# Kernel tuning notes

Measured on AMD Instinct MI355X. Metric: run time of the kernel, lower is better.

Reference implementation:

```python
import jax, jax.numpy as jnp
import numpy as np

B, S, D, H, F = 4, 1024, 1024, 16, 4096
DH = D // H
EPS = 1e-6


def _layer_norm(x, gamma, beta):
    # torch LayerNorm here uses unbiased std (ddof=1) and eps added to std
    mean = jnp.mean(x, axis=-1, keepdims=True)
    std = jnp.std(x, axis=-1, keepdims=True, ddof=1)
    return gamma * (x - mean) / (std + EPS) + beta


def _conv1d(x, w, b):
    # x: [B,S,C]; w: [out,in,3]; pad 'both' -> (1,1), same length
    y = jax.lax.conv_general_dilated(
        jnp.transpose(x, (0, 2, 1)), w, window_strides=(1,),
        padding=[(1, 1)], dimension_numbers=('NCH', 'OIH', 'NCH'))
    return jnp.transpose(y, (0, 2, 1)) + b


def setup_inputs() -> dict:
    key = jax.random.key(0)
    ks = jax.random.split(key, 8)
    sD = 1.0 / np.sqrt(D)
    sF = 1.0 / np.sqrt(F)
    return {
        'inputs': jax.random.normal(ks[0], (B, S, D), dtype=jnp.float32),
        'mask': jnp.zeros((B, 1, S), dtype=bool),
        'gamma1': jnp.ones((D,), jnp.float32),
        'beta1': jnp.zeros((D,), jnp.float32),
        'gamma2': jnp.ones((D,), jnp.float32),
        'beta2': jnp.zeros((D,), jnp.float32),
        'Wq': jax.random.normal(ks[1], (D, D), jnp.float32) * sD,
        'Wk': jax.random.normal(ks[2], (D, D), jnp.float32) * sD,
        'Wv': jax.random.normal(ks[3], (D, D), jnp.float32) * sD,
        'Wo': jax.random.normal(ks[4], (D, D), jnp.float32) * sD,
        'conv1_w': jax.random.normal(ks[5], (F, D, 3), jnp.float32) * sD,
        'conv1_b': jnp.zeros((F,), jnp.float32),
        'conv2_w': jax.random.normal(ks[6], (D, F, 3), jnp.float32) * sF,
        'conv2_b': jnp.zeros((D,), jnp.float32),
    }


def reference(inputs, mask, gamma1, beta1, gamma2, beta2, Wq, Wk, Wv, Wo,
              conv1_w, conv1_b, conv2_w, conv2_b):
    x = inputs
    x_norm = _layer_norm(x, gamma1, beta1)
    # projections (torch Linear, no bias): y = x @ W.T
    q = jnp.einsum('bsd,ed->bse', x_norm, Wq).reshape(B, S, H, DH).transpose(0, 2, 1, 3)
    k = jnp.einsum('bsd,ed->bse', x_norm, Wk).reshape(B, S, H, DH).transpose(0, 2, 1, 3)
    v = jnp.einsum('bsd,ed->bse', x_norm, Wv).reshape(B, S, H, DH).transpose(0, 2, 1, 3)
    q = q * (DH ** -0.5)
    logits = jnp.einsum('bhqd,bhkd->bhqk', q, k)  # [B,H,S,S]
    logits = jnp.where(mask[:, None, :, :], jnp.float32(-1e18), logits)
    weights = jax.nn.softmax(logits, axis=-1)
    ctx = jnp.einsum('bhqk,bhkd->bhqd', weights, v)
    ctx = ctx.transpose(0, 2, 1, 3).reshape(B, S, D)
    attn_out = jnp.einsum('bsd,ed->bse', ctx, Wo)
    x = x + attn_out  # layer dropout is identity at eval
    x_norm = _layer_norm(x, gamma2, beta2)
    # FFN 'cc': conv+relu applied after BOTH convs (source bug i<len always true)
    h = jax.nn.relu(_conv1d(x_norm, conv1_w, conv1_b))
    h = jax.nn.relu(_conv1d(h, conv2_w, conv2_b))
    return x + h
```

## Files before the change

### kernel.cpp

```cpp
#include <hip/hip_runtime.h>
#include <stdint.h>
#include <stddef.h>

typedef unsigned short u16;
typedef short short8 __attribute__((ext_vector_type(8)));
typedef float f32x4 __attribute__((ext_vector_type(4)));

#define B_ 4
#define S_ 1024
#define D_ 1024
#define H_ 16
#define F_ 4096
#define M_ 4096

__device__ __forceinline__ u16 f2bf(float f) {
  union { float f; unsigned u; } v; v.f = f;
  unsigned r = v.u + 0x7fffu + ((v.u >> 16) & 1u);
  return (u16)(r >> 16);
}
__device__ __forceinline__ float bf2f(u16 x) {
  union { unsigned u; float f; } v; v.u = ((unsigned)x) << 16; return v.f;
}

__device__ __forceinline__ void gld16(const u16* g, u16* l) {
  __builtin_amdgcn_global_load_lds(
      (__attribute__((address_space(1))) void*)g,
      (__attribute__((address_space(3))) void*)l, 16, 0, 0);
}

__global__ __launch_bounds__(256) void cvt_wqkvo(const float* __restrict__ q,
                                                 const float* __restrict__ k,
                                                 const float* __restrict__ v,
                                                 const float* __restrict__ o,
                                                 u16* __restrict__ d) {
  int i = blockIdx.x * 256 + threadIdx.x;
  int sel = i >> 18;
  const float* s = sel == 0 ? q : sel == 1 ? k : sel == 2 ? v : o;
  float sc = sel == 0 ? 0.125f : 1.0f;
  float4 val = *(const float4*)(s + (size_t)(i & 262143) * 4);
  unsigned lo = (unsigned)f2bf(val.x * sc) | ((unsigned)f2bf(val.y * sc) << 16);
  unsigned hi = (unsigned)f2bf(val.z * sc) | ((unsigned)f2bf(val.w * sc) << 16);
  *(uint2*)(d + (size_t)i * 4) = make_uint2(lo, hi);
}

__global__ __launch_bounds__(256) void pack3(const float* __restrict__ w,
                                             u16* __restrict__ d, int OUT, int IN) {
  int tot = OUT * IN;
  int i = blockIdx.x * blockDim.x + threadIdx.x;
  int stride = gridDim.x * blockDim.x;
  for (; i < tot; i += stride) {
#pragma unroll
    for (int t = 0; t < 3; ++t) d[(size_t)t * tot + i] = f2bf(w[(size_t)i * 3 + t]);
  }
}

__global__ __launch_bounds__(256) void layernorm(const float* __restrict__ x,
                                                 const float* __restrict__ g,
                                                 const float* __restrict__ be,
                                                 u16* __restrict__ out) {
  __shared__ float red[8];
  const int row = blockIdx.x, tid = threadIdx.x;
  const float* xr = x + (size_t)row * D_;
  float4 v = *(const float4*)(xr + tid * 4);
  float s = v.x + v.y + v.z + v.w;
  float q = v.x * v.x + v.y * v.y + v.z * v.z + v.w * v.w;
#pragma unroll
  for (int o = 32; o; o >>= 1) { s += __shfl_xor(s, o); q += __shfl_xor(q, o); }
  const int w = tid >> 6, lane = tid & 63;
  if (lane == 0) { red[w] = s; red[4 + w] = q; }
  __syncthreads();
  s = red[0] + red[1] + red[2] + red[3];
  q = red[4] + red[5] + red[6] + red[7];
  float mean = s * (1.f / 1024.f);
  float var = (q - 1024.f * mean * mean) * (1.f / 1023.f);
  var = fmaxf(var, 0.f);
  float r = 1.f / (sqrtf(var) + 1e-6f);
  const float* vv = &v.x;
  int c = tid * 4;
  unsigned lo = (unsigned)f2bf(g[c + 0] * (vv[0] - mean) * r + be[c + 0]) |
                ((unsigned)f2bf(g[c + 1] * (vv[1] - mean) * r + be[c + 1]) << 16);
  unsigned hi = (unsigned)f2bf(g[c + 2] * (vv[2] - mean) * r + be[c + 2]) |
                ((unsigned)f2bf(g[c + 3] * (vv[3] - mean) * r + be[c + 3]) << 16);
  *(uint2*)(out + (size_t)row * D_ + c) = make_uint2(lo, hi);
}

template <int MODE, int NN, int KK>
__device__ __forceinline__ void stage_half(int kt, int kind, const u16* __restrict__ Ag,
                                           const u16* __restrict__ Bg,
                                           const u16* __restrict__ zrow, int tapf,
                                           int m0, int n0, int tid,
                                           u16* AsB, u16* BsB) {
  const int buf = kt & 1;
  int tap, k0;
  if (MODE == 1) { tap = kt >> 4; k0 = (kt & 15) << 6; }
  else if (MODE == 2) { tap = tapf; k0 = kt << 6; }
  else { tap = 0; k0 = kt << 6; }
  const int gc = (tid & 7) ^ ((tid >> 3) & 7);
  if (kind >= 2) {
#pragma unroll
    for (int j = 0; j < 2; ++j) {
      int r = (kind - 2) * 64 + j * 128 + (tid >> 3);
      const u16* src;
      if (MODE == 0) {
        src = Ag + (size_t)(m0 + r) * KK + k0 + gc * 8;
      } else {
        int srow = (m0 & 1023) + r + tap - 1;
        src = ((unsigned)srow < 1024u)
                  ? Ag + (size_t)((m0 & ~1023) + srow) * KK + k0 + gc * 8
                  : zrow + k0 + gc * 8;
      }
      gld16(src, AsB + buf * 16384 + r * 64 + (tid & 7) * 8);
    }
  } else {
#pragma unroll
    for (int j = 0; j < 2; ++j) {
      int r = kind * 128 + j * 64 + (tid >> 3);
      const u16* src = Bg + (size_t)tap * NN * KK + (size_t)(n0 + r) * KK + k0 + gc * 8;
      gld16(src, BsB + buf * 16384 + r * 64 + (tid & 7) * 8);
    }
  }
}

template <int MODE, int NN, int KK, int NT>
__global__ __launch_bounds__(512, 2) void gemm256(const u16* __restrict__ Ag,
                                                  const u16* __restrict__ Bg,
                                                  const float* __restrict__ bias,
                                                  const u16* __restrict__ zrow,
                                                  u16* __restrict__ Cb) {
  __shared__ u16 As[2][256][64];
  __shared__ u16 Bs[2][256][64];
  const int tid = threadIdx.x;
  const int w = tid >> 6, lane = tid & 63;
  const int wr = w >> 2, wc = w & 3;

  const int bid = blockIdx.x;
  int wgid, mb, nb, tapf = 0;
  if (MODE == 1) wgid = (bid & 7) * 32 + (bid >> 3);
  else           wgid = (bid & 7) * 24 + (bid >> 3);
  if (MODE == 2) {
    mb = wgid & 15;
    int rest = wgid >> 4;
    tapf = rest >> 2;
    nb = rest & 3;
  } else {
    nb = wgid >> 4;
    mb = wgid & 15;
  }
  const int m0 = mb * 256, n0 = nb * 256;

  u16* AsB = &As[0][0][0];
  u16* BsB = &Bs[0][0][0];

  f32x4 acc[8][4] = {};

  stage_half<MODE, NN, KK>(0, 0, Ag, Bg, zrow, tapf, m0, n0, tid, AsB, BsB);
  stage_half<MODE, NN, KK>(0, 1, Ag, Bg, zrow, tapf, m0, n0, tid, AsB, BsB);
  stage_half<MODE, NN, KK>(0, 2, Ag, Bg, zrow, tapf, m0, n0, tid, AsB, BsB);
  stage_half<MODE, NN, KK>(0, 3, Ag, Bg, zrow, tapf, m0, n0, tid, AsB, BsB);
  stage_half<MODE, NN, KK>(1, 0, Ag, Bg, zrow, tapf, m0, n0, tid, AsB, BsB);
  stage_half<MODE, NN, KK>(1, 1, Ag, Bg, zrow, tapf, m0, n0, tid, AsB, BsB);
  stage_half<MODE, NN, KK>(1, 2, Ag, Bg, zrow, tapf, m0, n0, tid, AsB, BsB);
  asm volatile("s_waitcnt vmcnt(6)" ::: "memory");
  __builtin_amdgcn_s_barrier();

  for (int kt = 0; kt < NT; ++kt) {
    const int buf = kt & 1;
    short8 bF[4][2];
#pragma unroll
    for (int q = 0; q < 4; ++q) {
      short8 aF[2][2];
#pragma unroll
      for (int i = 0; i < 2; ++i)
#pragma unroll
        for (int kk = 0; kk < 2; ++kk) {
          int r = wr * 128 + (2 * q + i) * 16 + (lane & 15);
          int c = kk * 4 + (lane >> 4);
          aF[i][kk] = *(const short8*)&As[buf][r][(c ^ (r & 7)) * 8];
        }
      if (q == 0) {
#pragma unroll
        for (int ni = 0; ni < 4; ++ni)
#pragma unroll
          for (int kk = 0; kk < 2; ++kk) {
            int r = wc * 64 + ni * 16 + (lane & 15);
            int c = kk * 4 + (lane >> 4);
            bF[ni][kk] = *(const short8*)&Bs[buf][r][(c ^ (r & 7)) * 8];
          }
      }
      if (q == 0) { if (kt + 1 < NT) stage_half<MODE, NN, KK>(kt + 1, 3, Ag, Bg, zrow, tapf, m0, n0, tid, AsB, BsB); }
      else if (q == 1) { if (kt + 2 < NT) stage_half<MODE, NN, KK>(kt + 2, 0, Ag, Bg, zrow, tapf, m0, n0, tid, AsB, BsB); }
      else if (q == 2) { if (kt + 2 < NT) stage_half<MODE, NN, KK>(kt + 2, 1, Ag, Bg, zrow, tapf, m0, n0, tid, AsB, BsB); }
      else             { if (kt + 2 < NT) stage_half<MODE, NN, KK>(kt + 2, 2, Ag, Bg, zrow, tapf, m0, n0, tid, AsB, BsB); }
      if (q == 1) {
        if (kt + 2 < NT) asm volatile("s_waitcnt vmcnt(10)" ::: "memory");
        else             asm volatile("s_waitcnt vmcnt(0)" ::: "memory");
      } else if (q == 3) {
        if (kt + 2 < NT)      asm volatile("s_waitcnt vmcnt(8)" ::: "memory");
        else if (kt + 1 < NT) asm volatile("s_waitcnt vmcnt(2)" ::: "memory");
      }
      __builtin_amdgcn_s_barrier();
      asm volatile("s_waitcnt lgkmcnt(0)" ::: "memory");
      __builtin_amdgcn_sched_barrier(0);
      __builtin_amdgcn_s_setprio(1);
#pragma unroll
      for (int i = 0; i < 2; ++i)
#pragma unroll
        for (int ni = 0; ni < 4; ++ni)
#pragma unroll
          for (int kk = 0; kk < 2; ++kk)
            acc[2 * q + i][ni] = __builtin_amdgcn_mfma_f32_16x16x32_bf16(
                aF[i][kk], bF[ni][kk], acc[2 * q + i][ni], 0, 0, 0);
      __builtin_amdgcn_s_setprio(0);
      __builtin_amdgcn_s_barrier();
    }
  }

#pragma unroll
  for (int mi = 0; mi < 8; ++mi)
#pragma unroll
    for (int ni = 0; ni < 4; ++ni)
#pragma unroll
      for (int j = 0; j < 4; ++j) {
        int row = m0 + wr * 128 + mi * 16 + (lane >> 4) * 4 + j;
        int col = n0 + wc * 64 + ni * 16 + (lane & 15);
        float v = acc[mi][ni][j];
        if (MODE == 0) {
          Cb[(size_t)row * NN + col] = f2bf(v);
        } else if (MODE == 1) {
          Cb[(size_t)row * NN + col] = f2bf(fmaxf(v + bias[col], 0.f));
        } else {
          Cb[((size_t)tapf * 4096 + row) * NN + col] = f2bf(v);
        }
      }
}

template <int EPI, int NXB>
__global__ __launch_bounds__(256) void gemm_bt(const u16* __restrict__ A,
                                               const u16* __restrict__ Bm,
                                               int N, int K,
                                               void* __restrict__ C,
                                               const float* __restrict__ res) {
  __shared__ u16 As[128 * 64];
  __shared__ u16 Bs[128 * 64];
  const int tid = threadIdx.x;
  const int w = tid >> 6, lane = tid & 63;
  const int bid = blockIdx.x;
  const int idx = bid >> 3;
  const int xb = (bid & 7) * NXB + idx % NXB;
  const int yb = idx / NXB;
  const int m0 = yb * 128, n0 = xb * 128;
  const int wr = w >> 1, wc = w & 1;
  const int lrow = lane >> 3;
  const int swc = (lane & 7) ^ lrow;

  f32x4 acc[4][4] = {};

  for (int k0 = 0; k0 < K; k0 += 64) {
#pragma unroll
    for (int i = 0; i < 4; ++i) {
      int chunk = w * 4 + i;
      int row = chunk * 8 + lrow;
      gld16(A + (size_t)(m0 + row) * K + k0 + swc * 8, &As[chunk * 512]);
      gld16(Bm + (size_t)(n0 + row) * K + k0 + swc * 8, &Bs[chunk * 512]);
    }
    __syncthreads();
#pragma unroll
    for (int kk = 0; kk < 2; ++kk) {
      short8 aF[4], bF[4];
#pragma unroll
      for (int mi = 0; mi < 4; ++mi) {
        int row = wr * 64 + mi * 16 + (lane & 15);
        int ch = (kk * 4 + (lane >> 4)) ^ (row & 7);
        aF[mi] = *(const short8*)&As[row * 64 + ch * 8];
      }
#pragma unroll
      for (int ni = 0; ni < 4; ++ni) {
        int row = wc * 64 + ni * 16 + (lane & 15);
        int ch = (kk * 4 + (lane >> 4)) ^ (row & 7);
        bF[ni] = *(const short8*)&Bs[row * 64 + ch * 8];
      }
#pragma unroll
      for (int mi = 0; mi < 4; ++mi)
#pragma unroll
        for (int ni = 0; ni < 4; ++ni)
          acc[mi][ni] = __builtin_amdgcn_mfma_f32_16x16x32_bf16(aF[mi], bF[ni], acc[mi][ni], 0, 0, 0);
    }
    __syncthreads();
  }

#pragma unroll
  for (int mi = 0; mi < 4; ++mi)
#pragma unroll
    for (int ni = 0; ni < 4; ++ni)
#pragma unroll
      for (int j = 0; j < 4; ++j) {
        int row = m0 + wr * 64 + mi * 16 + (lane >> 4) * 4 + j;
        int col = n0 + wc * 64 + ni * 16 + (lane & 15);
        float v = acc[mi][ni][j];
        if (EPI == 0) ((u16*)C)[(size_t)row * N + col] = f2bf(v);
        else ((float*)C)[(size_t)row * N + col] = v + res[(size_t)row * N + col];
      }
}

__global__ __launch_bounds__(256) void conv2_reduce(const u16* __restrict__ P,
                                                    const float* __restrict__ bias,
                                                    const float* __restrict__ x2,
                                                    float* __restrict__ out) {
  size_t o = ((size_t)blockIdx.x * 256 + threadIdx.x) * 8;
  int col = (int)(o & 1023);
  short8 a = *(const short8*)(P + o);
  short8 b = *(const short8*)(P + 4194304 + o);
  short8 c = *(const short8*)(P + 8388608 + o);
  float4 r0 = *(const float4*)(x2 + o);
  float4 r1 = *(const float4*)(x2 + o + 4);
  float4 b0 = *(const float4*)(bias + col);
  float4 b1 = *(const float4*)(bias + col + 4);
  float4 o0, o1;
  const float* bb0 = &b0.x; const float* bb1 = &b1.x;
  float* p0 = &o0.x; float* p1 = &o1.x;
  const float* rr0 = &r0.x; const float* rr1 = &r1.x;
#pragma unroll
  for (int j = 0; j < 4; ++j) {
    float v = bf2f((u16)a[j]) + bf2f((u16)b[j]) + bf2f((u16)c[j]) + bb0[j];
    p0[j] = rr0[j] + fmaxf(v, 0.f);
  }
#pragma unroll
  for (int j = 0; j < 4; ++j) {
    float v = bf2f((u16)a[4 + j]) + bf2f((u16)b[4 + j]) + bf2f((u16)c[4 + j]) + bb1[j];
    p1[j] = rr1[j] + fmaxf(v, 0.f);
  }
  *(float4*)(out + o) = o0;
  *(float4*)(out + o + 4) = o1;
}

__global__ __launch_bounds__(256) void transpose_v(const u16* __restrict__ QKV,
                                                   u16* __restrict__ Vt) {
  __shared__ u16 T[64][72];
  const int tid = threadIdx.x;
  const int st = blockIdx.x, h = blockIdx.y, b = blockIdx.z;
  const int s0 = st * 64;
#pragma unroll
  for (int i = 0; i < 2; ++i) {
    int u = tid + i * 256;
    int s = u >> 3, c8 = u & 7;
    uint4 val = *(const uint4*)(QKV + (size_t)(b * 1024 + s0 + s) * 3072 + 2048 + h * 64 + c8 * 8);
    const u16* vp = (const u16*)&val;
#pragma unroll
    for (int k = 0; k < 8; ++k) T[s][c8 * 8 + k] = vp[k];
  }
  __syncthreads();
#pragma unroll
  for (int i = 0; i < 2; ++i) {
    int u = tid + i * 256;
    int d = u >> 3, c8 = u & 7;
    u16 tmp[8];
#pragma unroll
    for (int k = 0; k < 8; ++k) tmp[k] = T[c8 * 8 + k][d];
    uint4 o;
    o.x = (unsigned)tmp[0] | ((unsigned)tmp[1] << 16);
    o.y = (unsigned)tmp[2] | ((unsigned)tmp[3] << 16);
    o.z = (unsigned)tmp[4] | ((unsigned)tmp[5] << 16);
    o.w = (unsigned)tmp[6] | ((unsigned)tmp[7] << 16);
    *(uint4*)(Vt + (size_t)((b * 16 + h) * 64 + d) * 1024 + s0 + c8 * 8) = o;
  }
}

__global__ __launch_bounds__(256) void flash_attn(const u16* __restrict__ QKV,
                                                  const u16* __restrict__ Vt,
                                                  u16* __restrict__ Ctx) {
  __shared__ u16 Ks[64 * 64];
  __shared__ u16 Vs[64 * 64];
  __shared__ u16 Ps[4 * 16 * 64];
  const int tid = threadIdx.x;
  const int w = tid >> 6, lane = tid & 63;
  const int qt = blockIdx.x, h = blockIdx.y, b = blockIdx.z;
  const int q0 = qt * 64 + w * 16;
  const int lrow = lane >> 3;
  const int swc = (lane & 7) ^ lrow;

  short8 qF[2];
#pragma unroll
  for (int kk = 0; kk < 2; ++kk)
    qF[kk] = *(const short8*)(QKV + (size_t)(b * 1024 + q0 + (lane & 15)) * 3072 +
                              h * 64 + kk * 32 + (lane >> 4) * 8);

  float m_r[4], l_r[4];
  f32x4 accO[4] = {};
#pragma unroll
  for (int j = 0; j < 4; ++j) { m_r[j] = -1e30f; l_r[j] = 0.f; }

  for (int kt = 0; kt < 16; ++kt) {
#pragma unroll
    for (int i = 0; i < 2; ++i) {
      int chunk = w * 2 + i;
      int row = chunk * 8 + lrow;
      gld16(QKV + (size_t)(b * 1024 + kt * 64 + row) * 3072 + 1024 + h * 64 + swc * 8,
            &Ks[chunk * 512]);
      gld16(Vt + (size_t)((b * 16 + h) * 64 + row) * 1024 + kt * 64 + swc * 8, &Vs[chunk * 512]);
    }
    __syncthreads();

    f32x4 accS[4] = {};
#pragma unroll
    for (int nt = 0; nt < 4; ++nt) {
#pragma unroll
      for (int kk = 0; kk < 2; ++kk) {
        int row = nt * 16 + (lane & 15);
        int ch = (kk * 4 + (lane >> 4)) ^ (row & 7);
        short8 bF = *(const short8*)&Ks[row * 64 + ch * 8];
        accS[nt] = __builtin_amdgcn_mfma_f32_16x16x32_bf16(qF[kk], bF, accS[nt], 0, 0, 0);
      }
    }

#pragma unroll
    for (int j = 0; j < 4; ++j) {
      float mx = fmaxf(fmaxf(accS[0][j], accS[1][j]), fmaxf(accS[2][j], accS[3][j]));
#pragma unroll
      for (int o = 1; o < 16; o <<= 1) mx = fmaxf(mx, __shfl_xor(mx, o));
      float mnew = fmaxf(m_r[j], mx);
      int prow = (lane >> 4) * 4 + j;
      float s = 0.f;
#pragma unroll
      for (int nt = 0; nt < 4; ++nt) {
        float p = __expf(accS[nt][j] - mnew);
        s += p;
        int col = nt * 16 + (lane & 15);
        int ch = (col >> 3) ^ (prow & 7);
        Ps[w * 1024 + prow * 64 + ch * 8 + (col & 7)] = f2bf(p);
      }
#pragma unroll
      for (int o = 1; o < 16; o <<= 1) s += __shfl_xor(s, o);
      float alpha = __expf(m_r[j] - mnew);
      l_r[j] = l_r[j] * alpha + s;
      m_r[j] = mnew;
#pragma unroll
      for (int nt = 0; nt < 4; ++nt) accO[nt][j] *= alpha;
    }

#pragma unroll
    for (int kk = 0; kk < 2; ++kk) {
      int prow = lane & 15;
      int ch = (kk * 4 + (lane >> 4)) ^ (prow & 7);
      short8 aF = *(const short8*)&Ps[w * 1024 + prow * 64 + ch * 8];
#pragma unroll
      for (int nt = 0; nt < 4; ++nt) {
        int vrow = nt * 16 + (lane & 15);
        int vch = (kk * 4 + (lane >> 4)) ^ (vrow & 7);
        short8 bF = *(const short8*)&Vs[vrow * 64 + vch * 8];
        accO[nt] = __builtin_amdgcn_mfma_f32_16x16x32_bf16(aF, bF, accO[nt], 0, 0, 0);
      }
    }
    __syncthreads();
  }

#pragma unroll
  for (int nt = 0; nt < 4; ++nt)
#pragma unroll
    for (int j = 0; j < 4; ++j) {
      int row = q0 + (lane >> 4) * 4 + j;
      int col = h * 64 + nt * 16 + (lane & 15);
      Ctx[(size_t)(b * 1024 + row) * D_ + col] = f2bf(accO[nt][j] / l_r[j]);
    }
}

extern "C" void kernel_launch(void* const* d_in, const int* in_sizes, int n_in,
                              void* d_out, int out_size, void* d_ws, size_t ws_size,
                              hipStream_t stream) {
  const float* x_in = (const float*)d_in[0];
  const float* g1 = (const float*)d_in[2];
  const float* be1 = (const float*)d_in[3];
  const float* g2 = (const float*)d_in[4];
  const float* be2 = (const float*)d_in[5];
  const float* Wq = (const float*)d_in[6];
  const float* Wk = (const float*)d_in[7];
  const float* Wv = (const float*)d_in[8];
  const float* Wo = (const float*)d_in[9];
  const float* c1w = (const float*)d_in[10];
  const float* c1b = (const float*)d_in[11];
  const float* c2w = (const float*)d_in[12];
  const float* c2b = (const float*)d_in[13];
  float* out = (float*)d_out;
  char* ws = (char*)d_ws;

  const size_t OFF_WQKV = 0;
  const size_t OFF_WOB  = 6291456;
  const size_t OFF_W1T  = 8388608;
  const size_t OFF_W2T  = 33554432;
  const size_t OFF_XN1  = 58720256;
  const size_t OFF_QKV  = 67108864;
  const size_t OFF_H    = OFF_QKV;
  const size_t OFF_VT   = 100663296;
  const size_t OFF_X2   = 109051904;
  const size_t OFF_XN2  = 125829120;
  const size_t OFF_ZROW = 134217728;
  const size_t OFF_P    = 0;
  const size_t NEED     = 134225920;
  if (ws_size < NEED) return;

  u16* wqkv = (u16*)(ws + OFF_WQKV);
  u16* wo_b = (u16*)(ws + OFF_WOB);
  u16* w1t = (u16*)(ws + OFF_W1T);
  u16* w2t = (u16*)(ws + OFF_W2T);
  u16* xn1 = (u16*)(ws + OFF_XN1);
  u16* ctx = xn1;
  u16* qkv = (u16*)(ws + OFF_QKV);
  u16* hbuf = (u16*)(ws + OFF_H);
  u16* vt = (u16*)(ws + OFF_VT);
  float* x2 = (float*)(ws + OFF_X2);
  u16* xn2 = (u16*)(ws + OFF_XN2);
  u16* zrow = (u16*)(ws + OFF_ZROW);
  u16* part = (u16*)(ws + OFF_P);

  hipMemsetAsync(zrow, 0, 8192, stream);

  cvt_wqkvo<<<4096, 256, 0, stream>>>(Wq, Wk, Wv, Wo, wqkv);
  pack3<<<2048, 256, 0, stream>>>(c1w, w1t, F_, D_);
  pack3<<<2048, 256, 0, stream>>>(c2w, w2t, D_, F_);

  layernorm<<<M_, 256, 0, stream>>>(x_in, g1, be1, xn1);

  gemm256<0, 3072, 1024, 16><<<192, 512, 0, stream>>>(xn1, wqkv, nullptr, zrow, qkv);

  transpose_v<<<dim3(16, H_, B_), 256, 0, stream>>>(qkv, vt);

  flash_attn<<<dim3(16, H_, B_), 256, 0, stream>>>(qkv, vt, ctx);

  gemm_bt<1, 1><<<256, 256, 0, stream>>>(ctx, wo_b, 1024, 1024, x2, x_in);

  layernorm<<<M_, 256, 0, stream>>>(x2, g2, be2, xn2);

  gemm256<1, 4096, 1024, 48><<<256, 512, 0, stream>>>(xn2, w1t, c1b, zrow, hbuf);

  gemm256<2, 1024, 4096, 64><<<192, 512, 0, stream>>>(hbuf, w2t, nullptr, zrow, part);
  conv2_reduce<<<2048, 256, 0, stream>>>(part, c2b, x2, out);
}
```

Baseline: 383.8 us.

## Software-pipeline LDS fragment reads behind MFMA in GEMM main loop

Restructures the 256x256 GEMM main loop so each quarter-step issues its MFMAs on fragments already in registers, then prefetches the next quarter's A fragments (and the next tile's A/B fragments) from LDS, with double-buffered register fragments and the loop unrolled by two tiles. This hides LDS read latency behind matrix work and removes one barrier per quarter. It raises register pressure from the extra fragment buffers, adjusts the vmcnt wait thresholds, and assumes NT is even.

```diff
diff --git a/kernel.cpp b/kernel.cpp
--- a/kernel.cpp
+++ b/kernel.cpp
@@ -121,6 +121,70 @@
   }
 }
 
+__device__ __forceinline__ void read_a(const u16 (*Asb)[64], int wr, int lane,
+                                       int qn, short8 (&dst)[2][2]) {
+#pragma unroll
+  for (int i = 0; i < 2; ++i)
+#pragma unroll
+    for (int kk = 0; kk < 2; ++kk) {
+      int r = wr * 128 + (2 * qn + i) * 16 + (lane & 15);
+      int c = kk * 4 + (lane >> 4);
+      dst[i][kk] = *(const short8*)&Asb[r][(c ^ (r & 7)) * 8];
+    }
+}
+
+__device__ __forceinline__ void read_b(const u16 (*Bsb)[64], int wc, int lane,
+                                       short8 (&dst)[4][2]) {
+#pragma unroll
+  for (int ni = 0; ni < 4; ++ni)
+#pragma unroll
+    for (int kk = 0; kk < 2; ++kk) {
+      int r = wc * 64 + ni * 16 + (lane & 15);
+      int c = kk * 4 + (lane >> 4);
+      dst[ni][kk] = *(const short8*)&Bsb[r][(c ^ (r & 7)) * 8];
+    }
+}
+
+template <int MODE, int NN, int KK, int NT, int Q, int BUF, int TP>
+__device__ __forceinline__ void window(int T, u16 (&As)[2][256][64], u16 (&Bs)[2][256][64],
+                                       int wr, int wc, int lane, int tid,
+                                       const u16* __restrict__ Ag, const u16* __restrict__ Bg,
+                                       const u16* __restrict__ zrow, int tapf, int m0, int n0,
+                                       f32x4 (&acc)[8][4], short8 (&aC)[2][2],
+                                       short8 (&aN)[2][2], short8 (&bFr)[2][4][2]) {
+  __builtin_amdgcn_s_setprio(1);
+#pragma unroll
+  for (int i = 0; i < 2; ++i)
+#pragma unroll
+    for (int ni = 0; ni < 4; ++ni)
+#pragma unroll
+      for (int kk = 0; kk < 2; ++kk)
+        acc[2 * Q + i][ni] = __builtin_amdgcn_mfma_f32_16x16x32_bf16(
+            aC[i][kk], bFr[TP][ni][kk], acc[2 * Q + i][ni], 0, 0, 0);
+  __builtin_amdgcn_s_setprio(0);
+  if (Q == 1) {
+    if (T + 1 < NT) asm volatile("s_waitcnt vmcnt(8)" ::: "memory");
+    else            asm volatile("s_waitcnt vmcnt(0)" ::: "memory");
+  }
+  if (Q == 3 && T + 1 < NT) {
+    if (T + 2 < NT) asm volatile("s_waitcnt vmcnt(6)" ::: "memory");
+    else            asm volatile("s_waitcnt vmcnt(2)" ::: "memory");
+  }
+  if (Q < 3) {
+    read_a(As[BUF], wr, lane, Q + 1, aN);
+  } else if (T + 1 < NT) {
+    read_a(As[BUF ^ 1], wr, lane, 0, aN);
+    read_b(Bs[BUF ^ 1], wc, lane, bFr[TP ^ 1]);
+  }
+  if (Q == 0)      { if (T + 1 < NT) stage_half<MODE, NN, KK>(T + 1, 3, Ag, Bg, zrow, tapf, m0, n0, tid, &As[0][0][0], &Bs[0][0][0]); }
+  else if (Q == 1) { if (T + 2 < NT) stage_half<MODE, NN, KK>(T + 2, 0, Ag, Bg, zrow, tapf, m0, n0, tid, &As[0][0][0], &Bs[0][0][0]); }
+  else if (Q == 2) { if (T + 2 < NT) stage_half<MODE, NN, KK>(T + 2, 1, Ag, Bg, zrow, tapf, m0, n0, tid, &As[0][0][0], &Bs[0][0][0]); }
+  else             { if (T + 2 < NT) stage_half<MODE, NN, KK>(T + 2, 2, Ag, Bg, zrow, tapf, m0, n0, tid, &As[0][0][0], &Bs[0][0][0]); }
+  asm volatile("s_waitcnt lgkmcnt(0)" ::: "memory");
+  __builtin_amdgcn_sched_barrier(0);
+  __builtin_amdgcn_s_barrier();
+}
+
 template <int MODE, int NN, int KK, int NT>
 __global__ __launch_bounds__(512, 2) void gemm256(const u16* __restrict__ Ag,
                                                   const u16* __restrict__ Bg,
@@ -152,6 +216,8 @@
   u16* BsB = &Bs[0][0][0];
 
   f32x4 acc[8][4] = {};
+  short8 aP[2][2][2];
+  short8 bFr[2][4][2];
 
   stage_half<MODE, NN, KK>(0, 0, Ag, Bg, zrow, tapf, m0, n0, tid, AsB, BsB);
   stage_half<MODE, NN, KK>(0, 1, Ag, Bg, zrow, tapf, m0, n0, tid, AsB, BsB);
@@ -162,57 +228,21 @@
   stage_half<MODE, NN, KK>(1, 2, Ag, Bg, zrow, tapf, m0, n0, tid, AsB, BsB);
   asm volatile("s_waitcnt vmcnt(6)" ::: "memory");
   __builtin_amdgcn_s_barrier();
-
-  for (int kt = 0; kt < NT; ++kt) {
-    const int buf = kt & 1;
-    short8 bF[4][2];
-#pragma unroll
-    for (int q = 0; q < 4; ++q) {
-      short8 aF[2][2];
-#pragma unroll
-      for (int i = 0; i < 2; ++i)
-#pragma unroll
-        for (int kk = 0; kk < 2; ++kk) {
-          int r = wr * 128 + (2 * q + i) * 16 + (lane & 15);
-          int c = kk * 4 + (lane >> 4);
-          aF[i][kk] = *(const short8*)&As[buf][r][(c ^ (r & 7)) * 8];
-        }
-      if (q == 0) {
-#pragma unroll
-        for (int ni = 0; ni < 4; ++ni)
-#pragma unroll
-          for (int kk = 0; kk < 2; ++kk) {
-            int r = wc * 64 + ni * 16 + (lane & 15);
-            int c = kk * 4 + (lane >> 4);
-            bF[ni][kk] = *(const short8*)&Bs[buf][r][(c ^ (r & 7)) * 8];
-          }
-      }
-      if (q == 0) { if (kt + 1 < NT) stage_half<MODE, NN, KK>(kt + 1, 3, Ag, Bg, zrow, tapf, m0, n0, tid, AsB, BsB); }
-      else if (q == 1) { if (kt + 2 < NT) stage_half<MODE, NN, KK>(kt + 2, 0, Ag, Bg, zrow, tapf, m0, n0, tid, AsB, BsB); }
-      else if (q == 2) { if (kt + 2 < NT) stage_half<MODE, NN, KK>(kt + 2, 1, Ag, Bg, zrow, tapf, m0, n0, tid, AsB, BsB); }
-      else             { if (kt + 2 < NT) stage_half<MODE, NN, KK>(kt + 2, 2, Ag, Bg, zrow, tapf, m0, n0, tid, AsB, BsB); }
-      if (q == 1) {
-        if (kt + 2 < NT) asm volatile("s_waitcnt vmcnt(10)" ::: "memory");
-        else             asm volatile("s_waitcnt vmcnt(0)" ::: "memory");
-      } else if (q == 3) {
-        if (kt + 2 < NT)      asm volatile("s_waitcnt vmcnt(8)" ::: "memory");
-        else if (kt + 1 < NT) asm volatile("s_waitcnt vmcnt(2)" ::: "memory");
-      }
-      __builtin_amdgcn_s_barrier();
-      asm volatile("s_waitcnt lgkmcnt(0)" ::: "memory");
-      __builtin_amdgcn_sched_barrier(0);
-      __builtin_amdgcn_s_setprio(1);
-#pragma unroll
-      for (int i = 0; i < 2; ++i)
-#pragma unroll
-        for (int ni = 0; ni < 4; ++ni)
-#pragma unroll
-          for (int kk = 0; kk < 2; ++kk)
-            acc[2 * q + i][ni] = __builtin_amdgcn_mfma_f32_16x16x32_bf16(
-                aF[i][kk], bF[ni][kk], acc[2 * q + i][ni], 0, 0, 0);
-      __builtin_amdgcn_s_setprio(0);
-      __builtin_amdgcn_s_barrier();
-    }
+  read_a(As[0], wr, lane, 0, aP[0]);
+  read_b(Bs[0], wc, lane, bFr[0]);
+  asm volatile("s_waitcnt lgkmcnt(0)" ::: "memory");
+  __builtin_amdgcn_sched_barrier(0);
+
+  for (int it = 0; it < NT / 2; ++it) {
+    const int T0 = 2 * it;
+    window<MODE, NN, KK, NT, 0, 0, 0>(T0, As, Bs, wr, wc, lane, tid, Ag, Bg, zrow, tapf, m0, n0, acc, aP[0], aP[1], bFr);
+    window<MODE, NN, KK, NT, 1, 0, 0>(T0, As, Bs, wr, wc, lane, tid, Ag, Bg, zrow, tapf, m0, n0, acc, aP[1], aP[0], bFr);
+    window<MODE, NN, KK, NT, 2, 0, 0>(T0, As, Bs, wr, wc, lane, tid, Ag, Bg, zrow, tapf, m0, n0, acc, aP[0], aP[1], bFr);
+    window<MODE, NN, KK, NT, 3, 0, 0>(T0, As, Bs, wr, wc, lane, tid, Ag, Bg, zrow, tapf, m0, n0, acc, aP[1], aP[0], bFr);
+    window<MODE, NN, KK, NT, 0, 1, 1>(T0 + 1, As, Bs, wr, wc, lane, tid, Ag, Bg, zrow, tapf, m0, n0, acc, aP[0], aP[1], bFr);
+    window<MODE, NN, KK, NT, 1, 1, 1>(T0 + 1, As, Bs, wr, wc, lane, tid, Ag, Bg, zrow, tapf, m0, n0, acc, aP[1], aP[0], bFr);
+    window<MODE, NN, KK, NT, 2, 1, 1>(T0 + 1, As, Bs, wr, wc, lane, tid, Ag, Bg, zrow, tapf, m0, n0, acc, aP[0], aP[1], bFr);
+    window<MODE, NN, KK, NT, 3, 1, 1>(T0 + 1, As, Bs, wr, wc, lane, tid, Ag, Bg, zrow, tapf, m0, n0, acc, aP[1], aP[0], bFr);
   }
 
 #pragma unroll
```

Result: slower. 428.4 us (+11.6%).

## Restructure GEMM k-loop into two half-phases per tile with compile-time buffers

Applied to the files above, without the earlier changes.

The GEMM main loop drops from four quarter-steps per k-tile to two half-phases, each loading four A fragments and issuing 32 MFMAs between barriers. The loop is unrolled by two so the LDS buffer index is a compile-time constant. Three stage loads are grouped into the second phase and the vmcnt waits are retuned to match. This halves the barrier count per k-tile and lets more MFMAs issue per sync point, at the cost of more A-fragment registers and larger bursts of global loads.

```diff
diff --git a/kernel.cpp b/kernel.cpp
--- a/kernel.cpp
+++ b/kernel.cpp
@@ -121,6 +121,64 @@
   }
 }
 
+template <int MODE, int NN, int KK, int NT, int HF, int BUF>
+__device__ __forceinline__ void phase(int T, u16 (&As)[2][256][64], u16 (&Bs)[2][256][64],
+                                      int wr, int wc, int lane, int tid,
+                                      const u16* __restrict__ Ag, const u16* __restrict__ Bg,
+                                      const u16* __restrict__ zrow, int tapf, int m0, int n0,
+                                      f32x4 (&acc)[8][4], short8 (&aF)[4][2],
+                                      short8 (&bF)[4][2]) {
+#pragma unroll
+  for (int i = 0; i < 4; ++i)
+#pragma unroll
+    for (int kk = 0; kk < 2; ++kk) {
+      int r = wr * 128 + (4 * HF + i) * 16 + (lane & 15);
+      int c = kk * 4 + (lane >> 4);
+      aF[i][kk] = *(const short8*)&As[BUF][r][(c ^ (r & 7)) * 8];
+    }
+  if (HF == 0) {
+#pragma unroll
+    for (int ni = 0; ni < 4; ++ni)
+#pragma unroll
+      for (int kk = 0; kk < 2; ++kk) {
+        int r = wc * 64 + ni * 16 + (lane & 15);
+        int c = kk * 4 + (lane >> 4);
+        bF[ni][kk] = *(const short8*)&Bs[BUF][r][(c ^ (r & 7)) * 8];
+      }
+  }
+  if (HF == 0) {
+    if (T + 1 < NT)
+      stage_half<MODE, NN, KK>(T + 1, 3, Ag, Bg, zrow, tapf, m0, n0, tid, &As[0][0][0], &Bs[0][0][0]);
+  } else {
+    if (T + 2 < NT) {
+      stage_half<MODE, NN, KK>(T + 2, 0, Ag, Bg, zrow, tapf, m0, n0, tid, &As[0][0][0], &Bs[0][0][0]);
+      stage_half<MODE, NN, KK>(T + 2, 1, Ag, Bg, zrow, tapf, m0, n0, tid, &As[0][0][0], &Bs[0][0][0]);
+      stage_half<MODE, NN, KK>(T + 2, 2, Ag, Bg, zrow, tapf, m0, n0, tid, &As[0][0][0], &Bs[0][0][0]);
+    }
+  }
+  if (HF == 0) {
+    if (T + 1 < NT) asm volatile("s_waitcnt vmcnt(8)" ::: "memory");
+    else            asm volatile("s_waitcnt vmcnt(0)" ::: "memory");
+  } else {
+    if (T + 2 < NT)      asm volatile("s_waitcnt vmcnt(8)" ::: "memory");
+    else if (T + 1 < NT) asm volatile("s_waitcnt vmcnt(2)" ::: "memory");
+  }
+  __builtin_amdgcn_s_barrier();
+  asm volatile("s_waitcnt lgkmcnt(0)" ::: "memory");
+  __builtin_amdgcn_sched_barrier(0);
+  __builtin_amdgcn_s_setprio(1);
+#pragma unroll
+  for (int i = 0; i < 4; ++i)
+#pragma unroll
+    for (int ni = 0; ni < 4; ++ni)
+#pragma unroll
+      for (int kk = 0; kk < 2; ++kk)
+        acc[4 * HF + i][ni] = __builtin_amdgcn_mfma_f32_16x16x32_bf16(
+            aF[i][kk], bF[ni][kk], acc[4 * HF + i][ni], 0, 0, 0);
+  __builtin_amdgcn_s_setprio(0);
+  __builtin_amdgcn_s_barrier();
+}
+
 template <int MODE, int NN, int KK, int NT>
 __global__ __launch_bounds__(512, 2) void gemm256(const u16* __restrict__ Ag,
                                                   const u16* __restrict__ Bg,
@@ -152,6 +210,8 @@
   u16* BsB = &Bs[0][0][0];
 
   f32x4 acc[8][4] = {};
+  short8 aF[4][2];
+  short8 bF[4][2];
 
   stage_half<MODE, NN, KK>(0, 0, Ag, Bg, zrow, tapf, m0, n0, tid, AsB, BsB);
   stage_half<MODE, NN, KK>(0, 1, Ag, Bg, zrow, tapf, m0, n0, tid, AsB, BsB);
@@ -163,56 +223,12 @@
   asm volatile("s_waitcnt vmcnt(6)" ::: "memory");
   __builtin_amdgcn_s_barrier();
 
-  for (int kt = 0; kt < NT; ++kt) {
-    const int buf = kt & 1;
-    short8 bF[4][2];
-#pragma unroll
-    for (int q = 0; q < 4; ++q) {
-      short8 aF[2][2];
-#pragma unroll
-      for (int i = 0; i < 2; ++i)
-#pragma unroll
-        for (int kk = 0; kk < 2; ++kk) {
-          int r = wr * 128 + (2 * q + i) * 16 + (lane & 15);
-          int c = kk * 4 + (lane >> 4);
-          aF[i][kk] = *(const short8*)&As[buf][r][(c ^ (r & 7)) * 8];
-        }
-      if (q == 0) {
-#pragma unroll
-        for (int ni = 0; ni < 4; ++ni)
-#pragma unroll
-          for (int kk = 0; kk < 2; ++kk) {
-            int r = wc * 64 + ni * 16 + (lane & 15);
-            int c = kk * 4 + (lane >> 4);
-            bF[ni][kk] = *(const short8*)&Bs[buf][r][(c ^ (r & 7)) * 8];
-          }
-      }
-      if (q == 0) { if (kt + 1 < NT) stage_half<MODE, NN, KK>(kt + 1, 3, Ag, Bg, zrow, tapf, m0, n0, tid, AsB, BsB); }
-      else if (q == 1) { if (kt + 2 < NT) stage_half<MODE, NN, KK>(kt + 2, 0, Ag, Bg, zrow, tapf, m0, n0, tid, AsB, BsB); }
-      else if (q == 2) { if (kt + 2 < NT) stage_half<MODE, NN, KK>(kt + 2, 1, Ag, Bg, zrow, tapf, m0, n0, tid, AsB, BsB); }
-      else             { if (kt + 2 < NT) stage_half<MODE, NN, KK>(kt + 2, 2, Ag, Bg, zrow, tapf, m0, n0, tid, AsB, BsB); }
-      if (q == 1) {
-        if (kt + 2 < NT) asm volatile("s_waitcnt vmcnt(10)" ::: "memory");
-        else             asm volatile("s_waitcnt vmcnt(0)" ::: "memory");
-      } else if (q == 3) {
-        if (kt + 2 < NT)      asm volatile("s_waitcnt vmcnt(8)" ::: "memory");
-        else if (kt + 1 < NT) asm volatile("s_waitcnt vmcnt(2)" ::: "memory");
-      }
-      __builtin_amdgcn_s_barrier();
-      asm volatile("s_waitcnt lgkmcnt(0)" ::: "memory");
-      __builtin_amdgcn_sched_barrier(0);
-      __builtin_amdgcn_s_setprio(1);
-#pragma unroll
-      for (int i = 0; i < 2; ++i)
-#pragma unroll
-        for (int ni = 0; ni < 4; ++ni)
-#pragma unroll
-          for (int kk = 0; kk < 2; ++kk)
-            acc[2 * q + i][ni] = __builtin_amdgcn_mfma_f32_16x16x32_bf16(
-                aF[i][kk], bF[ni][kk], acc[2 * q + i][ni], 0, 0, 0);
-      __builtin_amdgcn_s_setprio(0);
-      __builtin_amdgcn_s_barrier();
-    }
+  for (int it = 0; it < NT / 2; ++it) {
+    const int T0 = 2 * it;
+    phase<MODE, NN, KK, NT, 0, 0>(T0, As, Bs, wr, wc, lane, tid, Ag, Bg, zrow, tapf, m0, n0, acc, aF, bF);
+    phase<MODE, NN, KK, NT, 1, 0>(T0, As, Bs, wr, wc, lane, tid, Ag, Bg, zrow, tapf, m0, n0, acc, aF, bF);
+    phase<MODE, NN, KK, NT, 0, 1>(T0 + 1, As, Bs, wr, wc, lane, tid, Ag, Bg, zrow, tapf, m0, n0, acc, aF, bF);
+    phase<MODE, NN, KK, NT, 1, 1>(T0 + 1, As, Bs, wr, wc, lane, tid, Ag, Bg, zrow, tapf, m0, n0, acc, aF, bF);
   }
 
 #pragma unroll
```

New measurement: 375.3 us. 1.02x faster.
